# Optimization experiments

Hardware: AMD Instinct MI355X
Metric: run time of the kernel (lower is better)

Reference implementation:

```python
import jax, jax.numpy as jnp
import numpy as np

D_IN = 128
D = 128
B, N = 2, 512
EPS = 1e-5


def _glorot(key, shape):
    fan_in = shape[-1]
    bound = 1.0 / np.sqrt(fan_in)
    return jax.random.uniform(key, shape, jnp.float32, -bound, bound)


def setup_inputs() -> dict:
    key = jax.random.key(0)
    ks = jax.random.split(key, 20)
    x = jax.random.normal(ks[0], (B, N, D_IN), jnp.float32)
    adj = jax.random.uniform(ks[1], (B, N, N), jnp.float32)
    return {
        "x": x,
        "adj": adj,
        # input linear
        "W_lin": _glorot(ks[2], (D, D_IN)), "b_lin": _glorot(ks[3], (D,)),
        # message network: Linear(D+1,D) -> ReLU -> Linear(D,D)
        "W_m1": _glorot(ks[4], (D, D + 1)), "b_m1": _glorot(ks[5], (D,)),
        "W_m2": _glorot(ks[6], (D, D)), "b_m2": _glorot(ks[7], (D,)),
        # DenseAtt: Linear(2D+1, 1) -> sigmoid
        "W_att": _glorot(ks[8], (1, 2 * D + 1)), "b_att": _glorot(ks[9], (1,)),
        # output network: Linear(D,D) -> ReLU -> Linear(D,D)
        "W_o1": _glorot(ks[10], (D, D)), "b_o1": _glorot(ks[11], (D,)),
        "W_o2": _glorot(ks[12], (D, D)), "b_o2": _glorot(ks[13], (D,)),
        # layernorm
        "ln_g": jnp.ones((D,), jnp.float32), "ln_b": jnp.zeros((D,), jnp.float32),
    }


def reference(x, adj, W_lin, b_lin, W_m1, b_m1, W_m2, b_m2,
              W_att, b_att, W_o1, b_o1, W_o2, b_o2, ln_g, ln_b):
    # input transform: [B,N,D]
    h = jnp.einsum('bnd,od->bno', x, W_lin) + b_lin
    b, n, d = h.shape
    adj_e = adj[..., None]                               # [B,N,N,1]
    h_right = jnp.broadcast_to(h[:, None, :, :], (b, n, n, d))  # neighbor features
    h_left = jnp.broadcast_to(h[:, :, None, :], (b, n, n, d))   # center features

    # message network on concat(h_right, adj): [B,N,N,D+1] -> [B,N,N,D]
    msg_in = jnp.concatenate([h_right, adj_e], axis=-1)
    m = jax.nn.relu(jnp.einsum('bnme,oe->bnmo', msg_in, W_m1) + b_m1)
    m = jnp.einsum('bnmd,od->bnmo', m, W_m2) + b_m2

    # dense attention: sigmoid(Linear(concat(h_left, h_right, adj)))
    att_in = jnp.concatenate([h_left, h_right, adj_e], axis=-1)  # [B,N,N,2D+1]
    att = jax.nn.sigmoid(jnp.einsum('bnme,oe->bnmo', att_in, W_att) + b_att)  # [B,N,N,1]

    # attention-weighted sum over neighbors (dim=2)
    agg = jnp.sum(m * att, axis=2)                       # [B,N,D]

    # output network
    agg = jax.nn.relu(jnp.einsum('bnd,od->bno', agg, W_o1) + b_o1)
    agg = jnp.einsum('bnd,od->bno', agg, W_o2) + b_o2

    u = h + agg
    # layernorm over last dim
    mu = jnp.mean(u, axis=-1, keepdims=True)
    var = jnp.mean(jnp.square(u - mu), axis=-1, keepdims=True)
    u = (u - mu) * jax.lax.rsqrt(var + EPS) * ln_g + ln_b
    out = jax.nn.relu(u)
    return out, adj
```

## Files before the change

kernel.cpp:

```cpp
#include <hip/hip_runtime.h>
#include <math.h>

#define NN 512
#define DD 128
#define ROWS 1024
#define NR 4

__device__ __forceinline__ float sigmoidf_(float z){ return 1.0f/(1.0f + __expf(-z)); }

__global__ __launch_bounds__(128) void k_rows(
    const float* __restrict__ x, const float* __restrict__ W_lin, const float* __restrict__ b_lin,
    const float* __restrict__ W_m1, const float* __restrict__ b_m1,
    const float* __restrict__ W_att,
    const float* __restrict__ W_m2, const float* __restrict__ W_o1, const float* __restrict__ W_o2,
    float* __restrict__ h, float* __restrict__ hm1,
    float* __restrict__ dotL, float* __restrict__ dotR,
    float* __restrict__ Wt_m2, float* __restrict__ Wt_o1, float* __restrict__ Wt_o2)
{
    const int r0 = blockIdx.x * NR;
    const int t  = threadIdx.x;
    __shared__ float xs[NR][DD];
    __shared__ float hs[NR][DD];
    __shared__ float red[2][2][NR];

    #pragma unroll
    for (int r = 0; r < NR; r++) xs[r][t] = x[(r0 + r) * DD + t];
    __syncthreads();

    float acc[NR];
    {
        float bl = b_lin[t];
        #pragma unroll
        for (int r = 0; r < NR; r++) acc[r] = bl;
        const float* wrow = W_lin + t * DD;
        for (int d = 0; d < DD; d += 4) {
            float4 w4 = *(const float4*)(wrow + d);
            #pragma unroll
            for (int r = 0; r < NR; r++) {
                float4 a4 = *(const float4*)(&xs[r][d]);
                acc[r] = fmaf(a4.x, w4.x, acc[r]);
                acc[r] = fmaf(a4.y, w4.y, acc[r]);
                acc[r] = fmaf(a4.z, w4.z, acc[r]);
                acc[r] = fmaf(a4.w, w4.w, acc[r]);
            }
        }
    }
    #pragma unroll
    for (int r = 0; r < NR; r++) { h[(r0 + r) * DD + t] = acc[r]; hs[r][t] = acc[r]; }

    {
        float wl = W_att[t], wr = W_att[DD + t];
        float pl[NR], pr[NR];
        #pragma unroll
        for (int r = 0; r < NR; r++) { pl[r] = acc[r] * wl; pr[r] = acc[r] * wr; }
        #pragma unroll
        for (int off = 32; off >= 1; off >>= 1) {
            #pragma unroll
            for (int r = 0; r < NR; r++) {
                pl[r] += __shfl_down(pl[r], off, 64);
                pr[r] += __shfl_down(pr[r], off, 64);
            }
        }
        int wid = t >> 6, lane = t & 63;
        if (lane == 0) {
            #pragma unroll
            for (int r = 0; r < NR; r++) { red[wid][0][r] = pl[r]; red[wid][1][r] = pr[r]; }
        }
    }
    __syncthreads();
    if (t < NR) {
        dotL[r0 + t] = red[0][0][t] + red[1][0][t];
        dotR[r0 + t] = red[0][1][t] + red[1][1][t];
    }

    {
        float acc2[NR];
        float bm = b_m1[t];
        #pragma unroll
        for (int r = 0; r < NR; r++) acc2[r] = bm;
        const float* wrow = W_m1 + t * (DD + 1);
        for (int d = 0; d < DD; d += 4) {
            float w0 = wrow[d], w1 = wrow[d+1], w2 = wrow[d+2], w3 = wrow[d+3];
            #pragma unroll
            for (int r = 0; r < NR; r++) {
                float4 a4 = *(const float4*)(&hs[r][d]);
                acc2[r] = fmaf(a4.x, w0, acc2[r]);
                acc2[r] = fmaf(a4.y, w1, acc2[r]);
                acc2[r] = fmaf(a4.z, w2, acc2[r]);
                acc2[r] = fmaf(a4.w, w3, acc2[r]);
            }
        }
        #pragma unroll
        for (int r = 0; r < NR; r++) hm1[(r0 + r) * DD + t] = acc2[r];
    }

    if (blockIdx.x < 48) {
        __shared__ float tlds[8][DD];
        const int w = blockIdx.x >> 4;
        const int s = blockIdx.x & 15;
        const float* src = (w == 0) ? W_m2 : (w == 1) ? W_o1 : W_o2;
        float*       dst = (w == 0) ? Wt_m2 : (w == 1) ? Wt_o1 : Wt_o2;
        #pragma unroll
        for (int j = 0; j < 8; j++) tlds[j][t] = src[(s * 8 + j) * DD + t];
        __syncthreads();
        float4 v0 = make_float4(tlds[0][t], tlds[1][t], tlds[2][t], tlds[3][t]);
        float4 v1 = make_float4(tlds[4][t], tlds[5][t], tlds[6][t], tlds[7][t]);
        *(float4*)(dst + t * DD + s * 8)     = v0;
        *(float4*)(dst + t * DD + s * 8 + 4) = v1;
    }
}

__global__ __launch_bounds__(512) void k_msgout(
    const float* __restrict__ adj, const float* __restrict__ hm1,
    const float* __restrict__ dotL, const float* __restrict__ dotR,
    const float* __restrict__ W_m1, const float* __restrict__ W_att, const float* __restrict__ b_att,
    const float* __restrict__ Wt_m2, const float* __restrict__ b_m2,
    const float* __restrict__ Wt_o1, const float* __restrict__ b_o1,
    const float* __restrict__ Wt_o2, const float* __restrict__ b_o2,
    const float* __restrict__ h, const float* __restrict__ ln_g, const float* __restrict__ ln_b,
    float* __restrict__ out, float* __restrict__ out_adj)
{
    const int r0   = blockIdx.x * NR;
    const int b    = r0 >> 9;
    const int t    = threadIdx.x;
    const int g    = t >> 6;
    const int lane = t & 63;
    const int rr   = t >> 7;
    const int o    = t & 127;
    const int oq   = t & 31;
    const int dg   = t >> 5;

    __shared__ float2 aa[NR][NN];
    __shared__ float2 red[8][NR][64];
    __shared__ float  pb[4][4][16][32];
    __shared__ float  vs[NR][DD];
    __shared__ float  vs2[NR][DD];
    __shared__ float2 wa1s[64];
    __shared__ float  satt[NR];
    __shared__ float  redsc[2][2][NR];

    if (t < 64)
        wa1s[t] = make_float2(W_m1[(2 * t) * (DD + 1) + DD],
                              W_m1[(2 * t + 1) * (DD + 1) + DD]);
    const float wAdj = W_att[2 * DD];
    const float bA   = b_att[0];

    {
        float drm = dotR[b * NN + t];
        #pragma unroll
        for (int i = 0; i < NR; i++) {
            float a = adj[(r0 + i) * NN + t];
            out_adj[(r0 + i) * NN + t] = a;
            float z = dotL[r0 + i] + drm + a * wAdj + bA;
            aa[i][t] = make_float2(a, sigmoidf_(z));
        }
    }
    __syncthreads();

    if (g < NR) {
        float s = 0.f;
        #pragma unroll
        for (int k = 0; k < 8; k++) s += aa[g][lane + 64 * k].y;
        #pragma unroll
        for (int off = 32; off >= 1; off >>= 1) s += __shfl_down(s, off, 64);
        if (lane == 0) satt[g] = s;
    }

    {
        float2 agg[NR];
        #pragma unroll
        for (int r = 0; r < NR; r++) agg[r] = make_float2(0.f, 0.f);
        float2 wa = wa1s[lane];
        const float* hbase = hm1 + (size_t)b * NN * DD + 2 * lane;
        #pragma unroll 4
        for (int m = g; m < NN; m += 8) {
            float2 hv = *(const float2*)(hbase + m * DD);
            #pragma unroll
            for (int r = 0; r < NR; r++) {
                float2 at = aa[r][m];
                float u0 = fmaxf(fmaf(at.x, wa.x, hv.x), 0.f);
                float u1 = fmaxf(fmaf(at.x, wa.y, hv.y), 0.f);
                agg[r].x = fmaf(at.y, u0, agg[r].x);
                agg[r].y = fmaf(at.y, u1, agg[r].y);
            }
        }
        #pragma unroll
        for (int r = 0; r < NR; r++) red[g][r][lane] = agg[r];
    }
    __syncthreads();
    {
        float s = 0.f;
        #pragma unroll
        for (int gg = 0; gg < 8; gg++)
            s += ((const float*)&red[gg][rr][0])[o];
        vs[rr][o] = s;
    }
    __syncthreads();

    {
        float a0[4], a1[4], a2[4], a3[4];
        #pragma unroll
        for (int r = 0; r < 4; r++) { a0[r]=0.f; a1[r]=0.f; a2[r]=0.f; a3[r]=0.f; }
        #pragma unroll
        for (int k = 0; k < 8; k++) {
            int d = dg * 8 + k;
            float4 w4 = *(const float4*)(Wt_m2 + d * DD + oq * 4);
            #pragma unroll
            for (int r = 0; r < 4; r++) {
                float xv = vs[r][d];
                a0[r] = fmaf(w4.x, xv, a0[r]);
                a1[r] = fmaf(w4.y, xv, a1[r]);
                a2[r] = fmaf(w4.z, xv, a2[r]);
                a3[r] = fmaf(w4.w, xv, a3[r]);
            }
        }
        #pragma unroll
        for (int r = 0; r < 4; r++) {
            pb[0][r][dg][oq] = a0[r]; pb[1][r][dg][oq] = a1[r];
            pb[2][r][dg][oq] = a2[r]; pb[3][r][dg][oq] = a3[r];
        }
    }
    __syncthreads();
    {
        float s = 0.f;
        #pragma unroll
        for (int d16 = 0; d16 < 16; d16++) s += pb[o & 3][rr][d16][o >> 2];
        vs2[rr][o] = s + b_m2[o] * satt[rr];
    }
    __syncthreads();

    {
        float a0[4], a1[4], a2[4], a3[4];
        #pragma unroll
        for (int r = 0; r < 4; r++) { a0[r]=0.f; a1[r]=0.f; a2[r]=0.f; a3[r]=0.f; }
        #pragma unroll
        for (int k = 0; k < 8; k++) {
            int d = dg * 8 + k;
            float4 w4 = *(const float4*)(Wt_o1 + d * DD + oq * 4);
            #pragma unroll
            for (int r = 0; r < 4; r++) {
                float xv = vs2[r][d];
                a0[r] = fmaf(w4.x, xv, a0[r]);
                a1[r] = fmaf(w4.y, xv, a1[r]);
                a2[r] = fmaf(w4.z, xv, a2[r]);
                a3[r] = fmaf(w4.w, xv, a3[r]);
            }
        }
        #pragma unroll
        for (int r = 0; r < 4; r++) {
            pb[0][r][dg][oq] = a0[r]; pb[1][r][dg][oq] = a1[r];
            pb[2][r][dg][oq] = a2[r]; pb[3][r][dg][oq] = a3[r];
        }
    }
    __syncthreads();
    {
        float s = 0.f;
        #pragma unroll
        for (int d16 = 0; d16 < 16; d16++) s += pb[o & 3][rr][d16][o >> 2];
        vs[rr][o] = fmaxf(s + b_o1[o], 0.f);
    }
    __syncthreads();

    {
        float a0[4], a1[4], a2[4], a3[4];
        #pragma unroll
        for (int r = 0; r < 4; r++) { a0[r]=0.f; a1[r]=0.f; a2[r]=0.f; a3[r]=0.f; }
        #pragma unroll
        for (int k = 0; k < 8; k++) {
            int d = dg * 8 + k;
            float4 w4 = *(const float4*)(Wt_o2 + d * DD + oq * 4);
            #pragma unroll
            for (int r = 0; r < 4; r++) {
                float xv = vs[r][d];
                a0[r] = fmaf(w4.x, xv, a0[r]);
                a1[r] = fmaf(w4.y, xv, a1[r]);
                a2[r] = fmaf(w4.z, xv, a2[r]);
                a3[r] = fmaf(w4.w, xv, a3[r]);
            }
        }
        #pragma unroll
        for (int r = 0; r < 4; r++) {
            pb[0][r][dg][oq] = a0[r]; pb[1][r][dg][oq] = a1[r];
            pb[2][r][dg][oq] = a2[r]; pb[3][r][dg][oq] = a3[r];
        }
    }
    __syncthreads();

    float v;
    {
        float s = 0.f;
        #pragma unroll
        for (int d16 = 0; d16 < 16; d16++) s += pb[o & 3][rr][d16][o >> 2];
        v = s + b_o2[o] + h[(r0 + rr) * DD + o];
    }

    {
        float p1 = v, p2 = v * v;
        #pragma unroll
        for (int off = 32; off >= 1; off >>= 1) {
            p1 += __shfl_down(p1, off, 64);
            p2 += __shfl_down(p2, off, 64);
        }
        int wid = (t >> 6) & 1;
        if ((t & 63) == 0) { redsc[wid][0][rr] = p1; redsc[wid][1][rr] = p2; }
    }
    __syncthreads();
    {
        float sum = redsc[0][0][rr] + redsc[1][0][rr];
        float sq  = redsc[0][1][rr] + redsc[1][1][rr];
        float mu  = sum * (1.0f / DD);
        float var = sq * (1.0f / DD) - mu * mu;
        float inv = rsqrtf(var + 1e-5f);
        out[(r0 + rr) * DD + o] = fmaxf(fmaf((v - mu) * inv, ln_g[o], ln_b[o]), 0.f);
    }
}

extern "C" void kernel_launch(void* const* d_in, const int* in_sizes, int n_in,
                              void* d_out, int out_size, void* d_ws, size_t ws_size,
                              hipStream_t stream)
{
    (void)in_sizes; (void)n_in; (void)out_size; (void)ws_size;
    const float* x     = (const float*)d_in[0];
    const float* adj   = (const float*)d_in[1];
    const float* W_lin = (const float*)d_in[2];
    const float* b_lin = (const float*)d_in[3];
    const float* W_m1  = (const float*)d_in[4];
    const float* b_m1  = (const float*)d_in[5];
    const float* W_m2  = (const float*)d_in[6];
    const float* b_m2  = (const float*)d_in[7];
    const float* W_att = (const float*)d_in[8];
    const float* b_att = (const float*)d_in[9];
    const float* W_o1  = (const float*)d_in[10];
    const float* b_o1  = (const float*)d_in[11];
    const float* W_o2  = (const float*)d_in[12];
    const float* b_o2  = (const float*)d_in[13];
    const float* ln_g  = (const float*)d_in[14];
    const float* ln_b  = (const float*)d_in[15];

    float* out     = (float*)d_out;
    float* out_adj = out + ROWS * DD;

    float* ws    = (float*)d_ws;
    float* hm1   = ws;
    float* dotL  = ws + 131072;
    float* dotR  = ws + 132096;
    float* h     = ws + 133120;
    float* Wt_m2 = ws + 264192;
    float* Wt_o1 = ws + 280576;
    float* Wt_o2 = ws + 296960;

    hipLaunchKernelGGL(k_rows, dim3(ROWS / NR), dim3(128), 0, stream,
                       x, W_lin, b_lin, W_m1, b_m1, W_att, W_m2, W_o1, W_o2,
                       h, hm1, dotL, dotR, Wt_m2, Wt_o1, Wt_o2);
    hipLaunchKernelGGL(k_msgout, dim3(ROWS / NR), dim3(512), 0, stream,
                       adj, hm1, dotL, dotR, W_m1, W_att, b_att,
                       Wt_m2, b_m2, Wt_o1, b_o1, Wt_o2, b_o2,
                       h, ln_g, ln_b, out, out_adj);
}
```

Before: 29.18 us.

## Fuse row and message kernels into one cooperative launch with grid sync

The two kernels become one cooperative kernel of 256 blocks x 512 threads, with a grid-wide barrier between the per-row linear stage and the message/output stage. The per-row GEMVs are split across 4 thread groups along the reduction dimension and summed through shared memory. h and dotL now stay in shared memory instead of round-tripping through global memory. This removes one kernel launch gap and some global traffic, at the cost of a grid sync and a cooperative-launch requirement that all blocks be co-resident.

```diff
diff --git a/kernel.cpp b/kernel.cpp
--- a/kernel.cpp
+++ b/kernel.cpp
@@ -1,158 +1,152 @@
 #include <hip/hip_runtime.h>
+#include <hip/hip_cooperative_groups.h>
 #include <math.h>
+
+namespace cg = cooperative_groups;
 
 #define NN 512
 #define DD 128
 #define ROWS 1024
 #define NR 4
+#define NBLK (ROWS/NR)
+#define NTHR 512
 
 __device__ __forceinline__ float sigmoidf_(float z){ return 1.0f/(1.0f + __expf(-z)); }
 
-__global__ __launch_bounds__(128) void k_rows(
-    const float* __restrict__ x, const float* __restrict__ W_lin, const float* __restrict__ b_lin,
+struct P1 {
+    float xs[NR][DD];
+    float pb2[4][NR][DD];
+};
+struct P23 {
+    float2 aa[NR][NN];
+    float2 red[8][NR][64];
+    float  pb[4][NR][16][32];
+    float  vs[NR][DD];
+    float  vs2[NR][DD];
+    float2 wa1s[64];
+};
+
+__global__ __launch_bounds__(NTHR) void fused(
+    const float* __restrict__ x, const float* __restrict__ adj,
+    const float* __restrict__ W_lin, const float* __restrict__ b_lin,
     const float* __restrict__ W_m1, const float* __restrict__ b_m1,
-    const float* __restrict__ W_att,
-    const float* __restrict__ W_m2, const float* __restrict__ W_o1, const float* __restrict__ W_o2,
-    float* __restrict__ h, float* __restrict__ hm1,
-    float* __restrict__ dotL, float* __restrict__ dotR,
+    const float* __restrict__ W_m2, const float* __restrict__ b_m2,
+    const float* __restrict__ W_att, const float* __restrict__ b_att,
+    const float* __restrict__ W_o1, const float* __restrict__ b_o1,
+    const float* __restrict__ W_o2, const float* __restrict__ b_o2,
+    const float* __restrict__ ln_g, const float* __restrict__ ln_b,
+    float* __restrict__ out, float* __restrict__ out_adj,
+    float* __restrict__ hm1g, float* __restrict__ dotRg,
     float* __restrict__ Wt_m2, float* __restrict__ Wt_o1, float* __restrict__ Wt_o2)
 {
-    const int r0 = blockIdx.x * NR;
-    const int t  = threadIdx.x;
-    __shared__ float xs[NR][DD];
+    const int r0   = blockIdx.x * NR;
+    const int b    = r0 >> 9;
+    const int t    = threadIdx.x;
+    const int rr   = t >> 7;
+    const int o    = t & 127;
+    const int q    = t >> 7;
+    const int g    = t >> 6;
+    const int lane = t & 63;
+
+    __shared__ __align__(16) unsigned char arena[sizeof(P23) > sizeof(P1) ? sizeof(P23) : sizeof(P1)];
+    P1&  p1 = *reinterpret_cast<P1*>(arena);
+    P23& p2 = *reinterpret_cast<P23*>(arena);
     __shared__ float hs[NR][DD];
-    __shared__ float red[2][2][NR];
-
-    #pragma unroll
-    for (int r = 0; r < NR; r++) xs[r][t] = x[(r0 + r) * DD + t];
-    __syncthreads();
-
-    float acc[NR];
-    {
-        float bl = b_lin[t];
-        #pragma unroll
-        for (int r = 0; r < NR; r++) acc[r] = bl;
-        const float* wrow = W_lin + t * DD;
-        for (int d = 0; d < DD; d += 4) {
-            float4 w4 = *(const float4*)(wrow + d);
+    __shared__ float dl[NR];
+    __shared__ float satt[NR];
+    __shared__ float redsc[2][2][NR];
+
+    ((float*)p1.xs)[t] = x[r0 * DD + t];
+    __syncthreads();
+
+    {
+        float a[NR] = {0.f, 0.f, 0.f, 0.f};
+        const float4* wp = (const float4*)(W_lin + o * DD + q * 32);
+        #pragma unroll
+        for (int k = 0; k < 8; k++) {
+            float4 w4 = wp[k];
+            int d = q * 32 + 4 * k;
             #pragma unroll
             for (int r = 0; r < NR; r++) {
-                float4 a4 = *(const float4*)(&xs[r][d]);
-                acc[r] = fmaf(a4.x, w4.x, acc[r]);
-                acc[r] = fmaf(a4.y, w4.y, acc[r]);
-                acc[r] = fmaf(a4.z, w4.z, acc[r]);
-                acc[r] = fmaf(a4.w, w4.w, acc[r]);
-            }
-        }
-    }
-    #pragma unroll
-    for (int r = 0; r < NR; r++) { h[(r0 + r) * DD + t] = acc[r]; hs[r][t] = acc[r]; }
-
-    {
-        float wl = W_att[t], wr = W_att[DD + t];
-        float pl[NR], pr[NR];
-        #pragma unroll
-        for (int r = 0; r < NR; r++) { pl[r] = acc[r] * wl; pr[r] = acc[r] * wr; }
-        #pragma unroll
-        for (int off = 32; off >= 1; off >>= 1) {
+                float4 xv = *(const float4*)&p1.xs[r][d];
+                a[r] = fmaf(xv.x, w4.x, a[r]);
+                a[r] = fmaf(xv.y, w4.y, a[r]);
+                a[r] = fmaf(xv.z, w4.z, a[r]);
+                a[r] = fmaf(xv.w, w4.w, a[r]);
+            }
+        }
+        #pragma unroll
+        for (int r = 0; r < NR; r++) p1.pb2[q][r][o] = a[r];
+    }
+    __syncthreads();
+    {
+        float hreg = b_lin[o] + p1.pb2[0][rr][o] + p1.pb2[1][rr][o]
+                              + p1.pb2[2][rr][o] + p1.pb2[3][rr][o];
+        hs[rr][o] = hreg;
+    }
+    __syncthreads();
+
+    {
+        int row = g & 3;
+        const float* wa = W_att + (g >> 2) * DD;
+        float p = hs[row][lane] * wa[lane] + hs[row][lane + 64] * wa[lane + 64];
+        #pragma unroll
+        for (int off = 32; off >= 1; off >>= 1) p += __shfl_down(p, off, 64);
+        if (lane == 0) {
+            if (g < 4) dl[row] = p;
+            else       dotRg[r0 + row] = p;
+        }
+    }
+
+    {
+        float a[NR] = {0.f, 0.f, 0.f, 0.f};
+        const float* w2 = W_m1 + o * (DD + 1) + q * 32;
+        #pragma unroll
+        for (int k = 0; k < 8; k++) {
+            int d = q * 32 + 4 * k;
+            float w0 = w2[4*k], w1 = w2[4*k+1], w2v = w2[4*k+2], w3 = w2[4*k+3];
             #pragma unroll
             for (int r = 0; r < NR; r++) {
-                pl[r] += __shfl_down(pl[r], off, 64);
-                pr[r] += __shfl_down(pr[r], off, 64);
-            }
-        }
-        int wid = t >> 6, lane = t & 63;
-        if (lane == 0) {
-            #pragma unroll
-            for (int r = 0; r < NR; r++) { red[wid][0][r] = pl[r]; red[wid][1][r] = pr[r]; }
-        }
-    }
-    __syncthreads();
-    if (t < NR) {
-        dotL[r0 + t] = red[0][0][t] + red[1][0][t];
-        dotR[r0 + t] = red[0][1][t] + red[1][1][t];
-    }
-
-    {
-        float acc2[NR];
-        float bm = b_m1[t];
-        #pragma unroll
-        for (int r = 0; r < NR; r++) acc2[r] = bm;
-        const float* wrow = W_m1 + t * (DD + 1);
-        for (int d = 0; d < DD; d += 4) {
-            float w0 = wrow[d], w1 = wrow[d+1], w2 = wrow[d+2], w3 = wrow[d+3];
-            #pragma unroll
-            for (int r = 0; r < NR; r++) {
-                float4 a4 = *(const float4*)(&hs[r][d]);
-                acc2[r] = fmaf(a4.x, w0, acc2[r]);
-                acc2[r] = fmaf(a4.y, w1, acc2[r]);
-                acc2[r] = fmaf(a4.z, w2, acc2[r]);
-                acc2[r] = fmaf(a4.w, w3, acc2[r]);
-            }
-        }
-        #pragma unroll
-        for (int r = 0; r < NR; r++) hm1[(r0 + r) * DD + t] = acc2[r];
-    }
-
-    if (blockIdx.x < 48) {
-        __shared__ float tlds[8][DD];
+                float4 xv = *(const float4*)&hs[r][d];
+                a[r] = fmaf(xv.x, w0,  a[r]);
+                a[r] = fmaf(xv.y, w1,  a[r]);
+                a[r] = fmaf(xv.z, w2v, a[r]);
+                a[r] = fmaf(xv.w, w3,  a[r]);
+            }
+        }
+        #pragma unroll
+        for (int r = 0; r < NR; r++) p1.pb2[q][r][o] = a[r];
+    }
+    __syncthreads();
+    hm1g[(r0 + rr) * DD + o] = b_m1[o] + p1.pb2[0][rr][o] + p1.pb2[1][rr][o]
+                                       + p1.pb2[2][rr][o] + p1.pb2[3][rr][o];
+
+    if (blockIdx.x < 48 && t < 128) {
         const int w = blockIdx.x >> 4;
         const int s = blockIdx.x & 15;
         const float* src = (w == 0) ? W_m2 : (w == 1) ? W_o1 : W_o2;
         float*       dst = (w == 0) ? Wt_m2 : (w == 1) ? Wt_o1 : Wt_o2;
         #pragma unroll
-        for (int j = 0; j < 8; j++) tlds[j][t] = src[(s * 8 + j) * DD + t];
-        __syncthreads();
-        float4 v0 = make_float4(tlds[0][t], tlds[1][t], tlds[2][t], tlds[3][t]);
-        float4 v1 = make_float4(tlds[4][t], tlds[5][t], tlds[6][t], tlds[7][t]);
-        *(float4*)(dst + t * DD + s * 8)     = v0;
-        *(float4*)(dst + t * DD + s * 8 + 4) = v1;
-    }
-}
-
-__global__ __launch_bounds__(512) void k_msgout(
-    const float* __restrict__ adj, const float* __restrict__ hm1,
-    const float* __restrict__ dotL, const float* __restrict__ dotR,
-    const float* __restrict__ W_m1, const float* __restrict__ W_att, const float* __restrict__ b_att,
-    const float* __restrict__ Wt_m2, const float* __restrict__ b_m2,
-    const float* __restrict__ Wt_o1, const float* __restrict__ b_o1,
-    const float* __restrict__ Wt_o2, const float* __restrict__ b_o2,
-    const float* __restrict__ h, const float* __restrict__ ln_g, const float* __restrict__ ln_b,
-    float* __restrict__ out, float* __restrict__ out_adj)
-{
-    const int r0   = blockIdx.x * NR;
-    const int b    = r0 >> 9;
-    const int t    = threadIdx.x;
-    const int g    = t >> 6;
-    const int lane = t & 63;
-    const int rr   = t >> 7;
-    const int o    = t & 127;
-    const int oq   = t & 31;
-    const int dg   = t >> 5;
-
-    __shared__ float2 aa[NR][NN];
-    __shared__ float2 red[8][NR][64];
-    __shared__ float  pb[4][4][16][32];
-    __shared__ float  vs[NR][DD];
-    __shared__ float  vs2[NR][DD];
-    __shared__ float2 wa1s[64];
-    __shared__ float  satt[NR];
-    __shared__ float  redsc[2][2][NR];
+        for (int j = 0; j < 8; j++)
+            dst[t * DD + s * 8 + j] = src[(s * 8 + j) * DD + t];
+    }
+
+    cg::this_grid().sync();
 
     if (t < 64)
-        wa1s[t] = make_float2(W_m1[(2 * t) * (DD + 1) + DD],
-                              W_m1[(2 * t + 1) * (DD + 1) + DD]);
+        p2.wa1s[t] = make_float2(W_m1[(2 * t) * (DD + 1) + DD],
+                                 W_m1[(2 * t + 1) * (DD + 1) + DD]);
     const float wAdj = W_att[2 * DD];
     const float bA   = b_att[0];
 
     {
-        float drm = dotR[b * NN + t];
+        float drm = dotRg[b * NN + t];
         #pragma unroll
         for (int i = 0; i < NR; i++) {
             float a = adj[(r0 + i) * NN + t];
             out_adj[(r0 + i) * NN + t] = a;
-            float z = dotL[r0 + i] + drm + a * wAdj + bA;
-            aa[i][t] = make_float2(a, sigmoidf_(z));
+            float z = dl[i] + drm + a * wAdj + bA;
+            p2.aa[i][t] = make_float2(a, sigmoidf_(z));
         }
     }
     __syncthreads();
@@ -160,7 +154,7 @@
     if (g < NR) {
         float s = 0.f;
         #pragma unroll
-        for (int k = 0; k < 8; k++) s += aa[g][lane + 64 * k].y;
+        for (int k = 0; k < 8; k++) s += p2.aa[g][lane + 64 * k].y;
         #pragma unroll
         for (int off = 32; off >= 1; off >>= 1) s += __shfl_down(s, off, 64);
         if (lane == 0) satt[g] = s;
@@ -170,14 +164,14 @@
         float2 agg[NR];
         #pragma unroll
         for (int r = 0; r < NR; r++) agg[r] = make_float2(0.f, 0.f);
-        float2 wa = wa1s[lane];
-        const float* hbase = hm1 + (size_t)b * NN * DD + 2 * lane;
+        float2 wa = p2.wa1s[lane];
+        const float* hbase = hm1g + (size_t)b * NN * DD + 2 * lane;
         #pragma unroll 4
         for (int m = g; m < NN; m += 8) {
             float2 hv = *(const float2*)(hbase + m * DD);
             #pragma unroll
             for (int r = 0; r < NR; r++) {
-                float2 at = aa[r][m];
+                float2 at = p2.aa[r][m];
                 float u0 = fmaxf(fmaf(at.x, wa.x, hv.x), 0.f);
                 float u1 = fmaxf(fmaf(at.x, wa.y, hv.y), 0.f);
                 agg[r].x = fmaf(at.y, u0, agg[r].x);
@@ -185,17 +179,20 @@
             }
         }
         #pragma unroll
-        for (int r = 0; r < NR; r++) red[g][r][lane] = agg[r];
+        for (int r = 0; r < NR; r++) p2.red[g][r][lane] = agg[r];
     }
     __syncthreads();
     {
         float s = 0.f;
         #pragma unroll
         for (int gg = 0; gg < 8; gg++)
-            s += ((const float*)&red[gg][rr][0])[o];
-        vs[rr][o] = s;
-    }
-    __syncthreads();
+            s += ((const float*)&p2.red[gg][rr][0])[o];
+        p2.vs[rr][o] = s;
+    }
+    __syncthreads();
+
+    const int oq = t & 31;
+    const int dg = t >> 5;
 
     {
         float a0[4], a1[4], a2[4], a3[4];
@@ -207,7 +204,7 @@
             float4 w4 = *(const float4*)(Wt_m2 + d * DD + oq * 4);
             #pragma unroll
             for (int r = 0; r < 4; r++) {
-                float xv = vs[r][d];
+                float xv = p2.vs[r][d];
                 a0[r] = fmaf(w4.x, xv, a0[r]);
                 a1[r] = fmaf(w4.y, xv, a1[r]);
                 a2[r] = fmaf(w4.z, xv, a2[r]);
@@ -216,16 +213,16 @@
         }
         #pragma unroll
         for (int r = 0; r < 4; r++) {
-            pb[0][r][dg][oq] = a0[r]; pb[1][r][dg][oq] = a1[r];
-            pb[2][r][dg][oq] = a2[r]; pb[3][r][dg][oq] = a3[r];
-        }
-    }
-    __syncthreads();
-    {
-        float s = 0.f;
-        #pragma unroll
-        for (int d16 = 0; d16 < 16; d16++) s += pb[o & 3][rr][d16][o >> 2];
-        vs2[rr][o] = s + b_m2[o] * satt[rr];
+            p2.pb[0][r][dg][oq] = a0[r]; p2.pb[1][r][dg][oq] = a1[r];
+            p2.pb[2][r][dg][oq] = a2[r]; p2.pb[3][r][dg][oq] = a3[r];
+        }
+    }
+    __syncthreads();
+    {
+        float s = 0.f;
+        #pragma unroll
+        for (int d16 = 0; d16 < 16; d16++) s += p2.pb[o & 3][rr][d16][o >> 2];
+        p2.vs2[rr][o] = s + b_m2[o] * satt[rr];
     }
     __syncthreads();
 
@@ -239,7 +236,7 @@
             float4 w4 = *(const float4*)(Wt_o1 + d * DD + oq * 4);
             #pragma unroll
             for (int r = 0; r < 4; r++) {
-                float xv = vs2[r][d];
+                float xv = p2.vs2[r][d];
                 a0[r] = fmaf(w4.x, xv, a0[r]);
                 a1[r] = fmaf(w4.y, xv, a1[r]);
                 a2[r] = fmaf(w4.z, xv, a2[r]);
@@ -248,16 +245,16 @@
         }
         #pragma unroll
         for (int r = 0; r < 4; r++) {
-            pb[0][r][dg][oq] = a0[r]; pb[1][r][dg][oq] = a1[r];
-            pb[2][r][dg][oq] = a2[r]; pb[3][r][dg][oq] = a3[r];
-        }
-    }
-    __syncthreads();
-    {
-        float s = 0.f;
-        #pragma unroll
-        for (int d16 = 0; d16 < 16; d16++) s += pb[o & 3][rr][d16][o >> 2];
-        vs[rr][o] = fmaxf(s + b_o1[o], 0.f);
+            p2.pb[0][r][dg][oq] = a0[r]; p2.pb[1][r][dg][oq] = a1[r];
+            p2.pb[2][r][dg][oq] = a2[r]; p2.pb[3][r][dg][oq] = a3[r];
+        }
+    }
+    __syncthreads();
+    {
+        float s = 0.f;
+        #pragma unroll
+        for (int d16 = 0; d16 < 16; d16++) s += p2.pb[o & 3][rr][d16][o >> 2];
+        p2.vs[rr][o] = fmaxf(s + b_o1[o], 0.f);
     }
     __syncthreads();
 
@@ -271,7 +268,7 @@
             float4 w4 = *(const float4*)(Wt_o2 + d * DD + oq * 4);
             #pragma unroll
             for (int r = 0; r < 4; r++) {
-                float xv = vs[r][d];
+                float xv = p2.vs[r][d];
                 a0[r] = fmaf(w4.x, xv, a0[r]);
                 a1[r] = fmaf(w4.y, xv, a1[r]);
                 a2[r] = fmaf(w4.z, xv, a2[r]);
@@ -280,8 +277,8 @@
         }
         #pragma unroll
         for (int r = 0; r < 4; r++) {
-            pb[0][r][dg][oq] = a0[r]; pb[1][r][dg][oq] = a1[r];
-            pb[2][r][dg][oq] = a2[r]; pb[3][r][dg][oq] = a3[r];
+            p2.pb[0][r][dg][oq] = a0[r]; p2.pb[1][r][dg][oq] = a1[r];
+            p2.pb[2][r][dg][oq] = a2[r]; p2.pb[3][r][dg][oq] = a3[r];
         }
     }
     __syncthreads();
@@ -290,19 +287,19 @@
     {
         float s = 0.f;
         #pragma unroll
-        for (int d16 = 0; d16 < 16; d16++) s += pb[o & 3][rr][d16][o >> 2];
-        v = s + b_o2[o] + h[(r0 + rr) * DD + o];
-    }
-
-    {
-        float p1 = v, p2 = v * v;
+        for (int d16 = 0; d16 < 16; d16++) s += p2.pb[o & 3][rr][d16][o >> 2];
+        v = s + b_o2[o] + hs[rr][o];
+    }
+
+    {
+        float p1v = v, p2v = v * v;
         #pragma unroll
         for (int off = 32; off >= 1; off >>= 1) {
-            p1 += __shfl_down(p1, off, 64);
-            p2 += __shfl_down(p2, off, 64);
+            p1v += __shfl_down(p1v, off, 64);
+            p2v += __shfl_down(p2v, off, 64);
         }
         int wid = (t >> 6) & 1;
-        if ((t & 63) == 0) { redsc[wid][0][rr] = p1; redsc[wid][1][rr] = p2; }
+        if ((t & 63) == 0) { redsc[wid][0][rr] = p1v; redsc[wid][1][rr] = p2v; }
     }
     __syncthreads();
     {
@@ -341,19 +338,25 @@
     float* out_adj = out + ROWS * DD;
 
     float* ws    = (float*)d_ws;
-    float* hm1   = ws;
-    float* dotL  = ws + 131072;
-    float* dotR  = ws + 132096;
-    float* h     = ws + 133120;
-    float* Wt_m2 = ws + 264192;
-    float* Wt_o1 = ws + 280576;
-    float* Wt_o2 = ws + 296960;
-
-    hipLaunchKernelGGL(k_rows, dim3(ROWS / NR), dim3(128), 0, stream,
-                       x, W_lin, b_lin, W_m1, b_m1, W_att, W_m2, W_o1, W_o2,
-                       h, hm1, dotL, dotR, Wt_m2, Wt_o1, Wt_o2);
-    hipLaunchKernelGGL(k_msgout, dim3(ROWS / NR), dim3(512), 0, stream,
-                       adj, hm1, dotL, dotR, W_m1, W_att, b_att,
-                       Wt_m2, b_m2, Wt_o1, b_o1, Wt_o2, b_o2,
-                       h, ln_g, ln_b, out, out_adj);
+    float* hm1g  = ws;
+    float* dotRg = ws + 131072;
+    float* Wt_m2 = ws + 132096;
+    float* Wt_o1 = ws + 148480;
+    float* Wt_o2 = ws + 164864;
+
+    void* args[] = {
+        (void*)&x, (void*)&adj,
+        (void*)&W_lin, (void*)&b_lin,
+        (void*)&W_m1, (void*)&b_m1,
+        (void*)&W_m2, (void*)&b_m2,
+        (void*)&W_att, (void*)&b_att,
+        (void*)&W_o1, (void*)&b_o1,
+        (void*)&W_o2, (void*)&b_o2,
+        (void*)&ln_g, (void*)&ln_b,
+        (void*)&out, (void*)&out_adj,
+        (void*)&hm1g, (void*)&dotRg,
+        (void*)&Wt_m2, (void*)&Wt_o1, (void*)&Wt_o2
+    };
+    hipLaunchCooperativeKernel((const void*)fused, dim3(NBLK), dim3(NTHR),
+                               args, 0, stream);
 }
```

Result: slower. 66.75 us (+128.8%).

## Split k_rows reductions across 512 threads with LDS partial-sum combine

Applied to the files above, without the earlier changes.

The row kernel now runs 512 threads instead of 128. Each group of 128 threads handles a quarter of the reduction dimension for the W_lin and W_m1 matvecs, and the partial sums are combined through shared memory. The attention dot products are handled one row per wavefront. The weight transpose now writes directly without an LDS staging buffer. The intent is to shorten the serial dependency chain of the first kernel and raise occupancy, in exchange for extra syncs, LDS traffic, and scalar uncoalesced transpose stores.

```diff
diff --git a/kernel.cpp b/kernel.cpp
--- a/kernel.cpp
+++ b/kernel.cpp
@@ -8,7 +8,7 @@
 
 __device__ __forceinline__ float sigmoidf_(float z){ return 1.0f/(1.0f + __expf(-z)); }
 
-__global__ __launch_bounds__(128) void k_rows(
+__global__ __launch_bounds__(512) void k_rows(
     const float* __restrict__ x, const float* __restrict__ W_lin, const float* __restrict__ b_lin,
     const float* __restrict__ W_m1, const float* __restrict__ b_m1,
     const float* __restrict__ W_att,
@@ -17,96 +17,92 @@
     float* __restrict__ dotL, float* __restrict__ dotR,
     float* __restrict__ Wt_m2, float* __restrict__ Wt_o1, float* __restrict__ Wt_o2)
 {
-    const int r0 = blockIdx.x * NR;
-    const int t  = threadIdx.x;
+    const int r0   = blockIdx.x * NR;
+    const int t    = threadIdx.x;
+    const int rr   = t >> 7;
+    const int o    = t & 127;
+    const int q    = t >> 7;
+    const int g    = t >> 6;
+    const int lane = t & 63;
+
     __shared__ float xs[NR][DD];
     __shared__ float hs[NR][DD];
-    __shared__ float red[2][2][NR];
-
-    #pragma unroll
-    for (int r = 0; r < NR; r++) xs[r][t] = x[(r0 + r) * DD + t];
-    __syncthreads();
-
-    float acc[NR];
-    {
-        float bl = b_lin[t];
-        #pragma unroll
-        for (int r = 0; r < NR; r++) acc[r] = bl;
-        const float* wrow = W_lin + t * DD;
-        for (int d = 0; d < DD; d += 4) {
-            float4 w4 = *(const float4*)(wrow + d);
+    __shared__ float pb2[4][NR][DD];
+
+    ((float*)xs)[t] = x[r0 * DD + t];
+    __syncthreads();
+
+    {
+        float a[NR] = {0.f, 0.f, 0.f, 0.f};
+        const float4* wp = (const float4*)(W_lin + o * DD + q * 32);
+        #pragma unroll
+        for (int k = 0; k < 8; k++) {
+            float4 w4 = wp[k];
+            int d = q * 32 + 4 * k;
             #pragma unroll
             for (int r = 0; r < NR; r++) {
-                float4 a4 = *(const float4*)(&xs[r][d]);
-                acc[r] = fmaf(a4.x, w4.x, acc[r]);
-                acc[r] = fmaf(a4.y, w4.y, acc[r]);
-                acc[r] = fmaf(a4.z, w4.z, acc[r]);
-                acc[r] = fmaf(a4.w, w4.w, acc[r]);
-            }
-        }
-    }
-    #pragma unroll
-    for (int r = 0; r < NR; r++) { h[(r0 + r) * DD + t] = acc[r]; hs[r][t] = acc[r]; }
-
-    {
-        float wl = W_att[t], wr = W_att[DD + t];
-        float pl[NR], pr[NR];
-        #pragma unroll
-        for (int r = 0; r < NR; r++) { pl[r] = acc[r] * wl; pr[r] = acc[r] * wr; }
-        #pragma unroll
-        for (int off = 32; off >= 1; off >>= 1) {
+                float4 xv = *(const float4*)&xs[r][d];
+                a[r] = fmaf(xv.x, w4.x, a[r]);
+                a[r] = fmaf(xv.y, w4.y, a[r]);
+                a[r] = fmaf(xv.z, w4.z, a[r]);
+                a[r] = fmaf(xv.w, w4.w, a[r]);
+            }
+        }
+        #pragma unroll
+        for (int r = 0; r < NR; r++) pb2[q][r][o] = a[r];
+    }
+    __syncthreads();
+    {
+        float hreg = b_lin[o] + pb2[0][rr][o] + pb2[1][rr][o]
+                              + pb2[2][rr][o] + pb2[3][rr][o];
+        hs[rr][o] = hreg;
+        h[(r0 + rr) * DD + o] = hreg;
+    }
+    __syncthreads();
+
+    {
+        int row = g & 3;
+        const float* wa = W_att + (g >> 2) * DD;
+        float p = hs[row][lane] * wa[lane] + hs[row][lane + 64] * wa[lane + 64];
+        #pragma unroll
+        for (int off = 32; off >= 1; off >>= 1) p += __shfl_down(p, off, 64);
+        if (lane == 0) {
+            if (g < 4) dotL[r0 + row] = p;
+            else       dotR[r0 + row] = p;
+        }
+    }
+
+    {
+        float a[NR] = {0.f, 0.f, 0.f, 0.f};
+        const float* w2 = W_m1 + o * (DD + 1) + q * 32;
+        #pragma unroll
+        for (int k = 0; k < 8; k++) {
+            int d = q * 32 + 4 * k;
+            float w0 = w2[4*k], w1 = w2[4*k+1], w2v = w2[4*k+2], w3 = w2[4*k+3];
             #pragma unroll
             for (int r = 0; r < NR; r++) {
-                pl[r] += __shfl_down(pl[r], off, 64);
-                pr[r] += __shfl_down(pr[r], off, 64);
-            }
-        }
-        int wid = t >> 6, lane = t & 63;
-        if (lane == 0) {
-            #pragma unroll
-            for (int r = 0; r < NR; r++) { red[wid][0][r] = pl[r]; red[wid][1][r] = pr[r]; }
-        }
-    }
-    __syncthreads();
-    if (t < NR) {
-        dotL[r0 + t] = red[0][0][t] + red[1][0][t];
-        dotR[r0 + t] = red[0][1][t] + red[1][1][t];
-    }
-
-    {
-        float acc2[NR];
-        float bm = b_m1[t];
-        #pragma unroll
-        for (int r = 0; r < NR; r++) acc2[r] = bm;
-        const float* wrow = W_m1 + t * (DD + 1);
-        for (int d = 0; d < DD; d += 4) {
-            float w0 = wrow[d], w1 = wrow[d+1], w2 = wrow[d+2], w3 = wrow[d+3];
-            #pragma unroll
-            for (int r = 0; r < NR; r++) {
-                float4 a4 = *(const float4*)(&hs[r][d]);
-                acc2[r] = fmaf(a4.x, w0, acc2[r]);
-                acc2[r] = fmaf(a4.y, w1, acc2[r]);
-                acc2[r] = fmaf(a4.z, w2, acc2[r]);
-                acc2[r] = fmaf(a4.w, w3, acc2[r]);
-            }
-        }
-        #pragma unroll
-        for (int r = 0; r < NR; r++) hm1[(r0 + r) * DD + t] = acc2[r];
-    }
-
-    if (blockIdx.x < 48) {
-        __shared__ float tlds[8][DD];
+                float4 xv = *(const float4*)&hs[r][d];
+                a[r] = fmaf(xv.x, w0,  a[r]);
+                a[r] = fmaf(xv.y, w1,  a[r]);
+                a[r] = fmaf(xv.z, w2v, a[r]);
+                a[r] = fmaf(xv.w, w3,  a[r]);
+            }
+        }
+        #pragma unroll
+        for (int r = 0; r < NR; r++) pb2[q][r][o] = a[r];
+    }
+    __syncthreads();
+    hm1[(r0 + rr) * DD + o] = b_m1[o] + pb2[0][rr][o] + pb2[1][rr][o]
+                                      + pb2[2][rr][o] + pb2[3][rr][o];
+
+    if (blockIdx.x < 48 && t < 128) {
         const int w = blockIdx.x >> 4;
         const int s = blockIdx.x & 15;
         const float* src = (w == 0) ? W_m2 : (w == 1) ? W_o1 : W_o2;
         float*       dst = (w == 0) ? Wt_m2 : (w == 1) ? Wt_o1 : Wt_o2;
         #pragma unroll
-        for (int j = 0; j < 8; j++) tlds[j][t] = src[(s * 8 + j) * DD + t];
-        __syncthreads();
-        float4 v0 = make_float4(tlds[0][t], tlds[1][t], tlds[2][t], tlds[3][t]);
-        float4 v1 = make_float4(tlds[4][t], tlds[5][t], tlds[6][t], tlds[7][t]);
-        *(float4*)(dst + t * DD + s * 8)     = v0;
-        *(float4*)(dst + t * DD + s * 8 + 4) = v1;
+        for (int j = 0; j < 8; j++)
+            dst[t * DD + s * 8 + j] = src[(s * 8 + j) * DD + t];
     }
 }
 
@@ -349,7 +345,7 @@
     float* Wt_o1 = ws + 280576;
     float* Wt_o2 = ws + 296960;
 
-    hipLaunchKernelGGL(k_rows, dim3(ROWS / NR), dim3(128), 0, stream,
+    hipLaunchKernelGGL(k_rows, dim3(ROWS / NR), dim3(512), 0, stream,
                        x, W_lin, b_lin, W_m1, b_m1, W_att, W_m2, W_o1, W_o2,
                        h, hm1, dotL, dotR, Wt_m2, Wt_o1, Wt_o2);
     hipLaunchKernelGGL(k_msgout, dim3(ROWS / NR), dim3(512), 0, stream,
```

Result: faster. 27.82 us (-4.7%).
